# Performance work log

Hardware: AMD Instinct MI355X
Metric: run time of the kernel (lower is better)

## Reference

```python
import jax, jax.numpy as jnp
import numpy as np

NUM_ITEMS = 10000
EMBED_DIM = 64
USER_PERSPECTIVE_IMPORTANCE = 0.5
LEAKY_SLOPE = 0.2
BATCH = 32
MAX_HIST = 200


def setup_inputs() -> dict:
    key = jax.random.key(0)
    k_ids, k_len, k_items, k_user, k_w, k_b = jax.random.split(key, 6)
    batch_history_ids = jax.random.randint(k_ids, (BATCH, MAX_HIST), 0, NUM_ITEMS, dtype=jnp.int32)
    # lengths must be >= 1 to avoid all-masked softmax rows
    batch_history_lengths = jnp.maximum(
        jax.random.randint(k_len, (BATCH,), 0, MAX_HIST, dtype=jnp.int32), 1)
    items_embedding = jax.random.normal(k_items, (NUM_ITEMS, EMBED_DIM), dtype=jnp.float32)
    user_embedding = jax.random.normal(k_user, (1, EMBED_DIM), dtype=jnp.float32)
    fc_weight = jax.random.normal(k_w, (EMBED_DIM, EMBED_DIM), dtype=jnp.float32) * (1.0 / np.sqrt(EMBED_DIM))
    fc_bias = jax.random.normal(k_b, (EMBED_DIM,), dtype=jnp.float32) * 0.01
    return {
        'batch_history_ids': batch_history_ids,
        'batch_history_lengths': batch_history_lengths,
        'items_embedding': items_embedding,
        'user_embedding': user_embedding,
        'fc_weight': fc_weight,
        'fc_bias': fc_bias,
    }


def reference(batch_history_ids, batch_history_lengths, items_embedding, user_embedding, fc_weight, fc_bias):
    # valid[b, n] = n < length[b]
    valid = jnp.arange(MAX_HIST)[None, :] < batch_history_lengths[:, None]  # [B, N]

    hist_emb = items_embedding[batch_history_ids]  # [B, N, F] ragged gather (padded)

    # item-perspective attention: [B, I, N]
    item_att = jnp.einsum('if,bnf->bin', items_embedding, hist_emb)
    # original adds -inf mask then leaky_relu; leaky_relu(-inf) = -inf -> softmax weight 0
    item_att = jnp.where(valid[:, None, :], jax.nn.leaky_relu(item_att, LEAKY_SLOPE), -jnp.inf)
    item_scores = jax.nn.softmax(item_att, axis=-1)  # [B, I, N]

    # user-perspective attention: constant across the item-query axis (q=1, repeated over I),
    # so compute once as [B, N] and broadcast (same math as 'qif,bnf->bqin').
    user_att = jnp.einsum('f,bnf->bn', user_embedding[0], hist_emb)
    user_att = jnp.where(valid, jax.nn.leaky_relu(user_att, LEAKY_SLOPE), -jnp.inf)
    user_scores = jax.nn.softmax(user_att, axis=-1)  # [B, N]

    w = USER_PERSPECTIVE_IMPORTANCE
    attn = (1.0 - w) * item_scores + w * user_scores[:, None, :]  # [B, I, N]

    personalized = jnp.einsum('bin,bnf->bif', attn, hist_emb)  # [B, I, F]
    projected = personalized @ fc_weight.T + fc_bias  # [B, I, F]
    # final per-item score: dot with item embedding
    return jnp.einsum('bif,if->bi', projected, items_embedding)  # [B, I]
```

## Files before the change

kernel.cpp:

```cpp
#include <hip/hip_runtime.h>
#include <hip/hip_bf16.h>
#include <math.h>

#define NUM_ITEMS 10000
#define EMBED_DIM 64
#define MAX_HIST 200
#define NPAD 208
#define BATCH 32
#define LEAKY 0.2f
#define W_USER 0.5f
#define LOG2E 1.4426950408889634f
#define ECLAMP 110.0f

typedef short bf16x8 __attribute__((ext_vector_type(8)));
typedef float f32x4 __attribute__((ext_vector_type(4)));

__device__ __forceinline__ unsigned short f2bf(float f) {
    __hip_bfloat16 h = __float2bfloat16(f);
    return __builtin_bit_cast(unsigned short, h);
}

__device__ __forceinline__ float fexp2(float x) {
#if __has_builtin(__builtin_amdgcn_exp2f)
    return __builtin_amdgcn_exp2f(x);
#else
    return exp2f(x);
#endif
}

__global__ __launch_bounds__(256) void prep_kernel(const int* __restrict__ ids,
                                                   const int* __restrict__ lens,
                                                   const float* __restrict__ items,
                                                   const float* __restrict__ user,
                                                   const float* __restrict__ W,
                                                   const float* __restrict__ bias,
                                                   unsigned short* __restrict__ items_att_bf,
                                                   unsigned short* __restrict__ wti_bf,
                                                   float* __restrict__ bdot,
                                                   unsigned short* __restrict__ hist_bf,
                                                   unsigned short* __restrict__ uh_bf) {
    const int tid = threadIdx.x;
    __shared__ float shW[EMBED_DIM * EMBED_DIM];
    __shared__ float red[8];
    __shared__ float sh_usf[NPAD];
    __shared__ float sh_uh[4][EMBED_DIM];

    if (blockIdx.x < NUM_ITEMS / 4) {
        for (int idx = tid; idx < EMBED_DIM * EMBED_DIM; idx += 256) shW[idx] = W[idx];
        __syncthreads();

        const int i = blockIdx.x * 4 + (tid >> 6);
        const int g = tid & 63;
        const float* irow = items + i * EMBED_DIM;

        float acc = 0.f;
#pragma unroll
        for (int f = 0; f < EMBED_DIM; ++f) acc += irow[f] * shW[f * EMBED_DIM + g];

        wti_bf[i * EMBED_DIM + g] = f2bf(acc);
        items_att_bf[i * EMBED_DIM + g] = f2bf(irow[g] * LOG2E);

        float bv = bias[g] * irow[g];
#pragma unroll
        for (int o = 32; o > 0; o >>= 1) bv += __shfl_xor(bv, o, 64);
        if (g == 0) bdot[i] = bv;
    } else {
        const int b = blockIdx.x - NUM_ITEMS / 4;

        for (int idx = tid; idx < NPAD * 8; idx += 256) {
            const int n = idx >> 3, q = idx & 7;
            bf16x8 v = (bf16x8)0;
            if (n < MAX_HIST) {
                const int id = ids[b * MAX_HIST + n];
                const float4* p = (const float4*)(items + id * EMBED_DIM + q * 8);
                float4 v0 = p[0], v1 = p[1];
                v[0] = (short)f2bf(v0.x); v[1] = (short)f2bf(v0.y);
                v[2] = (short)f2bf(v0.z); v[3] = (short)f2bf(v0.w);
                v[4] = (short)f2bf(v1.x); v[5] = (short)f2bf(v1.y);
                v[6] = (short)f2bf(v1.z); v[7] = (short)f2bf(v1.w);
            }
            *(bf16x8*)(hist_bf + (size_t)(b * NPAD + n) * EMBED_DIM + q * 8) = v;
        }

        const int len = lens[b];
        float s = -INFINITY;
        if (tid < len) {
            const int id = ids[b * MAX_HIST + tid];
            const float* h = items + id * EMBED_DIM;
            float a0 = 0.f, a1 = 0.f;
#pragma unroll
            for (int f = 0; f < EMBED_DIM; f += 2) {
                a0 += user[f] * h[f];
                a1 += user[f + 1] * h[f + 1];
            }
            float a = a0 + a1;
            s = fmaxf(a, LEAKY * a);
        }
        float m = s;
#pragma unroll
        for (int o = 32; o > 0; o >>= 1) m = fmaxf(m, __shfl_xor(m, o, 64));
        if ((tid & 63) == 0) red[tid >> 6] = m;
        __syncthreads();
        m = fmaxf(fmaxf(red[0], red[1]), fmaxf(red[2], red[3]));

        float e = (tid < len) ? __expf(s - m) : 0.f;
        float t = e;
#pragma unroll
        for (int o = 32; o > 0; o >>= 1) t += __shfl_xor(t, o, 64);
        if ((tid & 63) == 0) red[4 + (tid >> 6)] = t;
        __syncthreads();
        const float sum = red[4] + red[5] + red[6] + red[7];

        if (tid < NPAD) sh_usf[tid] = (tid < len) ? (e / sum) : 0.f;
        __syncthreads();

        const int f = tid & 63;
        const int part = tid >> 6;
        float uhp = 0.f;
        for (int n = part; n < len; n += 4)
            uhp += sh_usf[n] * items[(size_t)ids[b * MAX_HIST + n] * EMBED_DIM + f];
        sh_uh[part][f] = uhp;
        __syncthreads();
        if (tid < EMBED_DIM)
            uh_bf[b * EMBED_DIM + tid] =
                f2bf(sh_uh[0][tid] + sh_uh[1][tid] + sh_uh[2][tid] + sh_uh[3][tid]);
    }
}

__global__ __launch_bounds__(256) void main_kernel(const unsigned short* __restrict__ items_att_bf,
                                                   const unsigned short* __restrict__ wti_bf,
                                                   const float* __restrict__ bdot,
                                                   const unsigned short* __restrict__ hist_bf,
                                                   const unsigned short* __restrict__ uh_bf,
                                                   const int* __restrict__ lens,
                                                   float* __restrict__ out) {
    const int b = blockIdx.y;
    const int tid = threadIdx.x;
    const int lane = tid & 63;
    const int w = tid >> 6;

    __shared__ __align__(16) unsigned short sh_hist[NPAD * EMBED_DIM];

    const int len = lens[b];
    const int ntiles = (len + 15) >> 4;

    const float4* src = (const float4*)(hist_bf + (size_t)b * NPAD * EMBED_DIM);
    const int nf4 = ntiles * 16 * 8;
    for (int c = tid; c < nf4; c += 256) {
        const int n = c >> 3, q = c & 7;
        float4 v = src[c];
        const int byte = (n * 128 + q * 16) ^ ((n & 7) << 4);
        *(float4*)((char*)sh_hist + byte) = v;
    }
    __syncthreads();

    const int i0 = blockIdx.x * 64 + w * 16;
    if (i0 >= NUM_ITEMS) return;

    const int c16 = lane & 15;
    const int g = lane >> 4;
    const int i = i0 + c16;

    bf16x8 itf0 = *(const bf16x8*)(items_att_bf + (size_t)i * 64 + g * 8);
    bf16x8 itf1 = *(const bf16x8*)(items_att_bf + (size_t)i * 64 + 32 + g * 8);
    bf16x8 wtf0 = *(const bf16x8*)(wti_bf + (size_t)i * 64 + g * 8);
    bf16x8 wtf1 = *(const bf16x8*)(wti_bf + (size_t)i * 64 + 32 + g * 8);

    bf16x8 u0 = *(const bf16x8*)(uh_bf + b * 64 + g * 8);
    bf16x8 u1 = *(const bf16x8*)(uh_bf + b * 64 + 32 + g * 8);
    f32x4 suf = (f32x4)0.f;
    suf = __builtin_amdgcn_mfma_f32_16x16x32_bf16(u0, wtf0, suf, 0, 0, 0);
    suf = __builtin_amdgcn_mfma_f32_16x16x32_bf16(u1, wtf1, suf, 0, 0, 0);
    const float Su = suf[0];

    float Se = 0.f, Sh = 0.f;

#define TILE_BODY(T, MASKED)                                                              \
    {                                                                                     \
        const int n = (T) * 16 + c16;                                                     \
        const int base = n * 128, sw = (n & 7) << 4;                                      \
        bf16x8 a0 = *(const bf16x8*)((const char*)sh_hist + ((base + g * 16) ^ sw));      \
        bf16x8 a1 = *(const bf16x8*)((const char*)sh_hist + ((base + 64 + g * 16) ^ sw)); \
        f32x4 S = (f32x4)0.f, H = (f32x4)0.f;                                             \
        S = __builtin_amdgcn_mfma_f32_16x16x32_bf16(a0, itf0, S, 0, 0, 0);                \
        S = __builtin_amdgcn_mfma_f32_16x16x32_bf16(a1, itf1, S, 0, 0, 0);                \
        H = __builtin_amdgcn_mfma_f32_16x16x32_bf16(a0, wtf0, H, 0, 0, 0);                \
        H = __builtin_amdgcn_mfma_f32_16x16x32_bf16(a1, wtf1, H, 0, 0, 0);                \
        const int nb = (T) * 16 + g * 4;                                                  \
        float s0 = fmaxf(S[0], LEAKY * S[0]);                                             \
        float s1 = fmaxf(S[1], LEAKY * S[1]);                                             \
        float s2 = fmaxf(S[2], LEAKY * S[2]);                                             \
        float s3 = fmaxf(S[3], LEAKY * S[3]);                                             \
        if (MASKED) {                                                                     \
            s0 = (nb + 0 < len) ? s0 : -INFINITY;                                         \
            s1 = (nb + 1 < len) ? s1 : -INFINITY;                                         \
            s2 = (nb + 2 < len) ? s2 : -INFINITY;                                         \
            s3 = (nb + 3 < len) ? s3 : -INFINITY;                                         \
        }                                                                                 \
        const float e0 = fexp2(fminf(s0, ECLAMP)), e1 = fexp2(fminf(s1, ECLAMP));         \
        const float e2 = fexp2(fminf(s2, ECLAMP)), e3 = fexp2(fminf(s3, ECLAMP));         \
        Se += (e0 + e1) + (e2 + e3);                                                      \
        Sh = fmaf(e0, H[0], fmaf(e1, H[1], fmaf(e2, H[2], fmaf(e3, H[3], Sh))));          \
    }

    for (int t = 0; t < ntiles - 1; ++t) TILE_BODY(t, 0)
    TILE_BODY(ntiles - 1, 1)
#undef TILE_BODY

    Se += __shfl_xor(Se, 16, 64); Se += __shfl_xor(Se, 32, 64);
    Sh += __shfl_xor(Sh, 16, 64); Sh += __shfl_xor(Sh, 32, 64);

    if (g == 0)
        out[(size_t)b * NUM_ITEMS + i] =
            (1.0f - W_USER) * (Sh / Se) + W_USER * Su + bdot[i];
}

extern "C" void kernel_launch(void* const* d_in, const int* in_sizes, int n_in,
                              void* d_out, int out_size, void* d_ws, size_t ws_size,
                              hipStream_t stream) {
    const int* ids = (const int*)d_in[0];
    const int* lens = (const int*)d_in[1];
    const float* items = (const float*)d_in[2];
    const float* user = (const float*)d_in[3];
    const float* W = (const float*)d_in[4];
    const float* bias = (const float*)d_in[5];
    float* out = (float*)d_out;

    char* p = (char*)d_ws;
    unsigned short* items_att_bf = (unsigned short*)p; p += (size_t)NUM_ITEMS * EMBED_DIM * 2;
    unsigned short* wti_bf       = (unsigned short*)p; p += (size_t)NUM_ITEMS * EMBED_DIM * 2;
    float* bdot                  = (float*)p;          p += (size_t)NUM_ITEMS * 4;
    unsigned short* hist_bf      = (unsigned short*)p; p += (size_t)BATCH * NPAD * EMBED_DIM * 2;
    unsigned short* uh_bf        = (unsigned short*)p; p += (size_t)BATCH * EMBED_DIM * 2;

    prep_kernel<<<NUM_ITEMS / 4 + BATCH, 256, 0, stream>>>(ids, lens, items, user, W, bias,
                                                           items_att_bf, wti_bf, bdot,
                                                           hist_bf, uh_bf);

    dim3 grid((NUM_ITEMS + 63) / 64, BATCH);
    main_kernel<<<grid, 256, 0, stream>>>(items_att_bf, wti_bf, bdot, hist_bf, uh_bf, lens, out);
}
```

Before: 45.76 us.

## Process two item tiles per wave to reuse history fragments and halve staging

Each wave now scores 32 items (two 16-item MFMA tiles) against every history tile, so each LDS history fragment feeds eight MFMAs instead of four. The grid shrinks to half as many blocks, which halves the redundant copies of the batch history into LDS. Item and weight fragment loads are issued before the LDS staging so their global latency overlaps it. The next history tile is prefetched from LDS while the current epilogue runs. The cost is higher register pressure and a tail block that does more wasted work past the last item.

Result: slower. 47.45 us (+3.7%).

```diff
diff --git a/kernel.cpp b/kernel.cpp
--- a/kernel.cpp
+++ b/kernel.cpp
@@ -144,6 +144,23 @@
     const int len = lens[b];
     const int ntiles = (len + 15) >> 4;
 
+    const int c16 = lane & 15;
+    const int g = lane >> 4;
+    const int i0 = blockIdx.x * 128 + w * 32;
+    const int iA = i0 + c16;
+    const int iB = i0 + 16 + c16;
+
+    bf16x8 itfA0 = *(const bf16x8*)(items_att_bf + (size_t)iA * 64 + g * 8);
+    bf16x8 itfA1 = *(const bf16x8*)(items_att_bf + (size_t)iA * 64 + 32 + g * 8);
+    bf16x8 wtfA0 = *(const bf16x8*)(wti_bf + (size_t)iA * 64 + g * 8);
+    bf16x8 wtfA1 = *(const bf16x8*)(wti_bf + (size_t)iA * 64 + 32 + g * 8);
+    bf16x8 itfB0 = *(const bf16x8*)(items_att_bf + (size_t)iB * 64 + g * 8);
+    bf16x8 itfB1 = *(const bf16x8*)(items_att_bf + (size_t)iB * 64 + 32 + g * 8);
+    bf16x8 wtfB0 = *(const bf16x8*)(wti_bf + (size_t)iB * 64 + g * 8);
+    bf16x8 wtfB1 = *(const bf16x8*)(wti_bf + (size_t)iB * 64 + 32 + g * 8);
+    bf16x8 u0 = *(const bf16x8*)(uh_bf + b * 64 + g * 8);
+    bf16x8 u1 = *(const bf16x8*)(uh_bf + b * 64 + 32 + g * 8);
+
     const float4* src = (const float4*)(hist_bf + (size_t)b * NPAD * EMBED_DIM);
     const int nf4 = ntiles * 16 * 8;
     for (int c = tid; c < nf4; c += 256) {
@@ -154,65 +171,93 @@
     }
     __syncthreads();
 
-    const int i0 = blockIdx.x * 64 + w * 16;
     if (i0 >= NUM_ITEMS) return;
 
-    const int c16 = lane & 15;
-    const int g = lane >> 4;
-    const int i = i0 + c16;
-
-    bf16x8 itf0 = *(const bf16x8*)(items_att_bf + (size_t)i * 64 + g * 8);
-    bf16x8 itf1 = *(const bf16x8*)(items_att_bf + (size_t)i * 64 + 32 + g * 8);
-    bf16x8 wtf0 = *(const bf16x8*)(wti_bf + (size_t)i * 64 + g * 8);
-    bf16x8 wtf1 = *(const bf16x8*)(wti_bf + (size_t)i * 64 + 32 + g * 8);
-
-    bf16x8 u0 = *(const bf16x8*)(uh_bf + b * 64 + g * 8);
-    bf16x8 u1 = *(const bf16x8*)(uh_bf + b * 64 + 32 + g * 8);
-    f32x4 suf = (f32x4)0.f;
-    suf = __builtin_amdgcn_mfma_f32_16x16x32_bf16(u0, wtf0, suf, 0, 0, 0);
-    suf = __builtin_amdgcn_mfma_f32_16x16x32_bf16(u1, wtf1, suf, 0, 0, 0);
-    const float Su = suf[0];
-
-    float Se = 0.f, Sh = 0.f;
-
-#define TILE_BODY(T, MASKED)                                                              \
-    {                                                                                     \
-        const int n = (T) * 16 + c16;                                                     \
-        const int base = n * 128, sw = (n & 7) << 4;                                      \
-        bf16x8 a0 = *(const bf16x8*)((const char*)sh_hist + ((base + g * 16) ^ sw));      \
-        bf16x8 a1 = *(const bf16x8*)((const char*)sh_hist + ((base + 64 + g * 16) ^ sw)); \
-        f32x4 S = (f32x4)0.f, H = (f32x4)0.f;                                             \
-        S = __builtin_amdgcn_mfma_f32_16x16x32_bf16(a0, itf0, S, 0, 0, 0);                \
-        S = __builtin_amdgcn_mfma_f32_16x16x32_bf16(a1, itf1, S, 0, 0, 0);                \
-        H = __builtin_amdgcn_mfma_f32_16x16x32_bf16(a0, wtf0, H, 0, 0, 0);                \
-        H = __builtin_amdgcn_mfma_f32_16x16x32_bf16(a1, wtf1, H, 0, 0, 0);                \
-        const int nb = (T) * 16 + g * 4;                                                  \
-        float s0 = fmaxf(S[0], LEAKY * S[0]);                                             \
-        float s1 = fmaxf(S[1], LEAKY * S[1]);                                             \
-        float s2 = fmaxf(S[2], LEAKY * S[2]);                                             \
-        float s3 = fmaxf(S[3], LEAKY * S[3]);                                             \
-        if (MASKED) {                                                                     \
-            s0 = (nb + 0 < len) ? s0 : -INFINITY;                                         \
-            s1 = (nb + 1 < len) ? s1 : -INFINITY;                                         \
-            s2 = (nb + 2 < len) ? s2 : -INFINITY;                                         \
-            s3 = (nb + 3 < len) ? s3 : -INFINITY;                                         \
-        }                                                                                 \
-        const float e0 = fexp2(fminf(s0, ECLAMP)), e1 = fexp2(fminf(s1, ECLAMP));         \
-        const float e2 = fexp2(fminf(s2, ECLAMP)), e3 = fexp2(fminf(s3, ECLAMP));         \
-        Se += (e0 + e1) + (e2 + e3);                                                      \
-        Sh = fmaf(e0, H[0], fmaf(e1, H[1], fmaf(e2, H[2], fmaf(e3, H[3], Sh))));          \
-    }
-
-    for (int t = 0; t < ntiles - 1; ++t) TILE_BODY(t, 0)
-    TILE_BODY(ntiles - 1, 1)
-#undef TILE_BODY
-
-    Se += __shfl_xor(Se, 16, 64); Se += __shfl_xor(Se, 32, 64);
-    Sh += __shfl_xor(Sh, 16, 64); Sh += __shfl_xor(Sh, 32, 64);
-
-    if (g == 0)
-        out[(size_t)b * NUM_ITEMS + i] =
-            (1.0f - W_USER) * (Sh / Se) + W_USER * Su + bdot[i];
+    f32x4 sufA = (f32x4)0.f, sufB = (f32x4)0.f;
+    sufA = __builtin_amdgcn_mfma_f32_16x16x32_bf16(u0, wtfA0, sufA, 0, 0, 0);
+    sufA = __builtin_amdgcn_mfma_f32_16x16x32_bf16(u1, wtfA1, sufA, 0, 0, 0);
+    sufB = __builtin_amdgcn_mfma_f32_16x16x32_bf16(u0, wtfB0, sufB, 0, 0, 0);
+    sufB = __builtin_amdgcn_mfma_f32_16x16x32_bf16(u1, wtfB1, sufB, 0, 0, 0);
+    const float SuA = sufA[0];
+    const float SuB = sufB[0];
+
+    float SeA = 0.f, ShA = 0.f, SeB = 0.f, ShB = 0.f;
+
+    const char* hbase = (const char*)sh_hist;
+#define LDA(T, X0, X1)                                                   \
+    {                                                                    \
+        const int n_ = (T) * 16 + c16;                                   \
+        const int base_ = n_ * 128, sw_ = (n_ & 7) << 4;                 \
+        X0 = *(const bf16x8*)(hbase + ((base_ + g * 16) ^ sw_));         \
+        X1 = *(const bf16x8*)(hbase + ((base_ + 64 + g * 16) ^ sw_));    \
+    }
+
+#define EPI(S, H, Se, Sh, MASKED, NB)                                    \
+    {                                                                    \
+        float s0 = fminf(fmaxf(S[0], LEAKY * S[0]), ECLAMP);             \
+        float s1 = fminf(fmaxf(S[1], LEAKY * S[1]), ECLAMP);             \
+        float s2 = fminf(fmaxf(S[2], LEAKY * S[2]), ECLAMP);             \
+        float s3 = fminf(fmaxf(S[3], LEAKY * S[3]), ECLAMP);             \
+        if (MASKED) {                                                    \
+            s0 = ((NB) + 0 < len) ? s0 : -INFINITY;                      \
+            s1 = ((NB) + 1 < len) ? s1 : -INFINITY;                      \
+            s2 = ((NB) + 2 < len) ? s2 : -INFINITY;                      \
+            s3 = ((NB) + 3 < len) ? s3 : -INFINITY;                      \
+        }                                                                \
+        const float e0 = fexp2(s0), e1 = fexp2(s1);                      \
+        const float e2 = fexp2(s2), e3 = fexp2(s3);                      \
+        Se += (e0 + e1) + (e2 + e3);                                     \
+        Sh = fmaf(e0, H[0], fmaf(e1, H[1], fmaf(e2, H[2], fmaf(e3, H[3], Sh)))); \
+    }
+
+#define MFMA8(A0, A1, SA, HA, SB, HB)                                     \
+    SA = __builtin_amdgcn_mfma_f32_16x16x32_bf16(A0, itfA0, SA, 0, 0, 0); \
+    SA = __builtin_amdgcn_mfma_f32_16x16x32_bf16(A1, itfA1, SA, 0, 0, 0); \
+    SB = __builtin_amdgcn_mfma_f32_16x16x32_bf16(A0, itfB0, SB, 0, 0, 0); \
+    SB = __builtin_amdgcn_mfma_f32_16x16x32_bf16(A1, itfB1, SB, 0, 0, 0); \
+    HA = __builtin_amdgcn_mfma_f32_16x16x32_bf16(A0, wtfA0, HA, 0, 0, 0); \
+    HA = __builtin_amdgcn_mfma_f32_16x16x32_bf16(A1, wtfA1, HA, 0, 0, 0); \
+    HB = __builtin_amdgcn_mfma_f32_16x16x32_bf16(A0, wtfB0, HB, 0, 0, 0); \
+    HB = __builtin_amdgcn_mfma_f32_16x16x32_bf16(A1, wtfB1, HB, 0, 0, 0);
+
+    bf16x8 a0, a1;
+    LDA(0, a0, a1)
+
+    for (int t = 0; t < ntiles - 1; ++t) {
+        f32x4 SA = (f32x4)0.f, HA = (f32x4)0.f, SB = (f32x4)0.f, HB = (f32x4)0.f;
+        MFMA8(a0, a1, SA, HA, SB, HB)
+        bf16x8 p0, p1;
+        LDA(t + 1, p0, p1)
+        const int nb = t * 16 + g * 4;
+        (void)nb;
+        EPI(SA, HA, SeA, ShA, 0, 0)
+        EPI(SB, HB, SeB, ShB, 0, 0)
+        a0 = p0; a1 = p1;
+    }
+    {
+        f32x4 SA = (f32x4)0.f, HA = (f32x4)0.f, SB = (f32x4)0.f, HB = (f32x4)0.f;
+        MFMA8(a0, a1, SA, HA, SB, HB)
+        const int nb = (ntiles - 1) * 16 + g * 4;
+        EPI(SA, HA, SeA, ShA, 1, nb)
+        EPI(SB, HB, SeB, ShB, 1, nb)
+    }
+#undef MFMA8
+#undef EPI
+#undef LDA
+
+    SeA += __shfl_xor(SeA, 16, 64); SeA += __shfl_xor(SeA, 32, 64);
+    ShA += __shfl_xor(ShA, 16, 64); ShA += __shfl_xor(ShA, 32, 64);
+    SeB += __shfl_xor(SeB, 16, 64); SeB += __shfl_xor(SeB, 32, 64);
+    ShB += __shfl_xor(ShB, 16, 64); ShB += __shfl_xor(ShB, 32, 64);
+
+    if (g == 0) {
+        if (iA < NUM_ITEMS)
+            out[(size_t)b * NUM_ITEMS + iA] =
+                (1.0f - W_USER) * (ShA / SeA) + W_USER * SuA + bdot[iA];
+        if (iB < NUM_ITEMS)
+            out[(size_t)b * NUM_ITEMS + iB] =
+                (1.0f - W_USER) * (ShB / SeB) + W_USER * SuB + bdot[iB];
+    }
 }
 
 extern "C" void kernel_launch(void* const* d_in, const int* in_sizes, int n_in,
@@ -237,6 +282,6 @@
                                                            items_att_bf, wti_bf, bdot,
                                                            hist_bf, uh_bf);
 
-    dim3 grid((NUM_ITEMS + 63) / 64, BATCH);
+    dim3 grid((NUM_ITEMS + 127) / 128, BATCH);
     main_kernel<<<grid, 256, 0, stream>>>(items_att_bf, wti_bf, bdot, hist_bf, uh_bf, lens, out);
 }
```
